# Performance work log

Hardware: AMD Instinct MI355X
Metric: run time of the kernel (lower is better)

The kernel has to match this reference:

```python
import jax, jax.numpy as jnp
import numpy as np

K = 16
H = 128

def _gelu(x):
    return jax.nn.gelu(x, approximate=False)  # torch nn.GELU default (erf)

def _knn_idx(xyz, k):
    # squared pairwise distances; topk of squared dist == topk of cdist (monotone)
    sq = jnp.sum(xyz * xyz, axis=-1)  # [B,N]
    d2 = sq[:, :, None] + sq[:, None, :] - 2.0 * jnp.einsum('bnd,bmd->bnm', xyz, xyz)
    n = xyz.shape[1]
    d2 = d2.at[:, jnp.arange(n), jnp.arange(n)].set(-1.0)  # force self first
    _, idx = jax.lax.top_k(-d2, min(k + 1, n))  # smallest distances
    return idx[..., 1:]  # drop self -> [B,N,K]

def _gather(feat, idx):
    # feat [B,N,C], idx [B,N,K] -> [B,N,K,C]
    return jax.vmap(lambda f, i: f[i])(feat, idx)

def setup_inputs() -> dict:
    key = jax.random.key(0)
    ks = jax.random.split(key, 13)
    s = 0.05
    return {
        'points': jax.random.normal(ks[0], (4, 4096, 6), jnp.float32),
        'Wc1': jax.random.normal(ks[1], (3, H), jnp.float32) * s,
        'bc1': jnp.zeros((H,), jnp.float32),
        'Wc2': jax.random.normal(ks[2], (H, H), jnp.float32) * s,
        'bc2': jnp.zeros((H,), jnp.float32),
        'Wn1': jax.random.normal(ks[3], (4, H), jnp.float32) * s,
        'bn1': jnp.zeros((H,), jnp.float32),
        'Wn2': jax.random.normal(ks[4], (H, H), jnp.float32) * s,
        'bn2': jnp.zeros((H,), jnp.float32),
        'Wo1': jax.random.normal(ks[5], (2 * H, H), jnp.float32) * s,
        'bo1': jnp.zeros((H,), jnp.float32),
        'Wo2': jax.random.normal(ks[6], (H, H), jnp.float32) * s,
        'bo2': jnp.zeros((H,), jnp.float32),
        'k': K,
    }

def reference(points, Wc1, bc1, Wc2, bc2, Wn1, bn1, Wn2, bn2, Wo1, bo1, Wo2, bo2, k):
    xyz = points[..., :3]
    normals = points[..., 3:6]
    idx = jax.lax.stop_gradient(_knn_idx(xyz, k))  # [B,N,K]

    # coord branch: relative neighbor coords -> MLP -> max over K
    rel_xyz = _gather(xyz, idx) - xyz[:, :, None, :]          # [B,N,K,3]
    h = _gelu(rel_xyz @ Wc1 + bc1) @ Wc2 + bc2                # [B,N,K,H]
    coord_feat = jnp.max(h, axis=2)                           # [B,N,H]

    # normal branch: neighbor normals + 1 - cos variation
    neigh_n = _gather(normals, idx)                           # [B,N,K,3]
    variation = 1.0 - jnp.sum(normals[:, :, None, :] * neigh_n, axis=-1, keepdims=True)
    nin = jnp.concatenate([neigh_n, variation], axis=-1)      # [B,N,K,4]
    g = _gelu(nin @ Wn1 + bn1) @ Wn2 + bn2                    # [B,N,K,H]
    normal_feat = jnp.max(g, axis=2)                          # [B,N,H]

    cat = jnp.concatenate([coord_feat, normal_feat], axis=-1) # [B,N,2H]
    return _gelu(cat @ Wo1 + bo1) @ Wo2 + bo2                 # [B,N,H]
```

## Files before the change

kernel.cpp:

```cpp
#include <hip/hip_runtime.h>
#include <math.h>

#define BATCH 4
#define NPTS 4096
#define KNBR 16
#define HDIM 128

typedef __attribute__((ext_vector_type(8))) short bf16x8;
typedef __attribute__((ext_vector_type(4))) float f32x4;
typedef unsigned long long u64;

#define WSOFF_W (1u << 20)
#define WC_HI 0
#define WC_LO 16384
#define WN_HI 32768
#define WN_LO 49152
#define WO1_HI 65536
#define WO1_LO 98304
#define WO2_HI 131072
#define WO2_LO 147456

__device__ __forceinline__ float gelu_f(float x) {
    const float z = x * 0.7071067811865476f;
    const float u = fabsf(z);
    const float z2 = z * z;
    const float t = __builtin_amdgcn_rcpf(fmaf(0.3275911f, u, 1.0f));
    const float E = __expf(-z2);
    float p = fmaf(t, 1.061405429f, -1.453152027f);
    p = fmaf(t, p, 1.421413741f);
    p = fmaf(t, p, -0.284496736f);
    p = fmaf(t, p, 0.254829592f);
    p = p * t;
    const float e = fmaf(-p, E, 1.0f);
    const float hx = 0.5f * x;
    return fmaf(fabsf(hx), e, hx);
}

__device__ __forceinline__ void bsplit(float x, short& hi, short& lo) {
    const unsigned u = __float_as_uint(x);
    hi = (short)(u >> 16);
    const float r = x - __uint_as_float(u & 0xffff0000u);
    lo = (short)(__float_as_uint(r) >> 16);
}

__device__ __forceinline__ u64 readlane_u64(u64 v, int src) {
    const unsigned lo = (unsigned)__builtin_amdgcn_readlane((int)(unsigned)v, src);
    const unsigned hi = (unsigned)__builtin_amdgcn_readlane((int)(unsigned)(v >> 32), src);
    return ((u64)hi << 32) | lo;
}

__global__ __launch_bounds__(256) void prep_points(const float* __restrict__ pts,
                                                   float4* __restrict__ ctab) {
    const int e = blockIdx.x * 256 + threadIdx.x;
    const float* __restrict__ p = pts + (size_t)e * 6;
    const float x = p[0], y = p[1], z = p[2];
    const float sq = x * x + y * y + z * z;
    ctab[e] = make_float4(x, y, z, sq);
}

__global__ __launch_bounds__(256) void prep_weights(
    const float* __restrict__ Wc2, const float* __restrict__ Wn2,
    const float* __restrict__ Wo1, const float* __restrict__ Wo2,
    unsigned short* __restrict__ wbuf)
{
    const int e = blockIdx.x * 256 + threadIdx.x;
    const float* src;
    unsigned short *dh, *dl;
    int idx;
    if (e < 16384)      { src = Wc2; dh = wbuf + WC_HI;  dl = wbuf + WC_LO;  idx = e; }
    else if (e < 32768) { src = Wn2; dh = wbuf + WN_HI;  dl = wbuf + WN_LO;  idx = e - 16384; }
    else if (e < 65536) { src = Wo1; dh = wbuf + WO1_HI; dl = wbuf + WO1_LO; idx = e - 32768; }
    else                { src = Wo2; dh = wbuf + WO2_HI; dl = wbuf + WO2_LO; idx = e - 65536; }
    const int j = idx & 7;
    const int l = (idx >> 3) & 63;
    const int tile = idx >> 9;
    const int ct = tile & 7;
    const int ks = tile >> 3;
    const int n = (l & 15) + 16 * ct;
    const int k = ks * 32 + ((l >> 4) << 3) + j;
    const float x = src[k * 128 + n];
    short hi, lo;
    bsplit(x, hi, lo);
    dh[idx] = (unsigned short)hi;
    dl[idx] = (unsigned short)lo;
}

__global__ __launch_bounds__(256) void knn_kernel(const float4* __restrict__ ctab,
                                                  int* __restrict__ idx_out) {
    const int wq = blockIdx.x * 4 + (threadIdx.x >> 6);
    const int b = wq >> 12;
    const int n = wq & (NPTS - 1);
    const int lane = threadIdx.x & 63;
    const float4* __restrict__ cb = ctab + (size_t)b * NPTS;

    const float4 q = cb[n];

    u64 run = ~0ull;
    u64 cur16max = ~0ull;

    for (int c = 0; c < NPTS / 64; ++c) {
        const int m = lane + 64 * c;
        const float4 cc = cb[m];
        const float dot = q.x * cc.x + q.y * cc.y + q.z * cc.z;
        float d2 = (q.w + cc.w) - 2.0f * dot;
        d2 = fmaxf(d2, 0.0f);
        u64 key = ((u64)__float_as_uint(d2) << 32) | (unsigned)m;
        if (m == n) key = ~0ull;

        u64 mask = __ballot(key < cur16max);
        while (mask) {
            const int src = (int)__builtin_ctzll(mask);
            const u64 K = readlane_u64(key, src);
            u64 prev = __shfl_up(run, 1, 64);
            if (lane == 0) prev = 0;
            run = (run < K) ? run : ((prev < K) ? K : prev);
            cur16max = readlane_u64(run, 15);
            mask &= mask - 1;
            mask &= __ballot(key < cur16max);
        }
    }

    if (lane < KNBR)
        idx_out[((size_t)b * NPTS + n) * KNBR + lane] = (int)(run & 0xffffffffull);
}

template<int NIN>
__device__ __forceinline__ void branch_compute(
    const float (* __restrict__ inp)[4],
    const float* __restrict__ w1s,
    const float* __restrict__ b1s,
    const float* __restrict__ b2s,
    const unsigned short* __restrict__ w2hi,
    const unsigned short* __restrict__ w2lo,
    unsigned short (* __restrict__ catH)[264],
    unsigned short (* __restrict__ catL)[264],
    int colbase, int w, int l)
{
    const int lr = l & 15;
    const int lq = l >> 4;
    const int kb = lq * 8;

    bf16x8 ah[4][2], al[4][2];
#pragma unroll
    for (int ks = 0; ks < 4; ++ks) {
        const int c0 = ks * 32 + kb;
        float wr[NIN][8], bb[8];
#pragma unroll
        for (int d = 0; d < NIN; ++d) {
            *(float4*)&wr[d][0] = *(const float4*)(w1s + (d << 7) + c0);
            *(float4*)&wr[d][4] = *(const float4*)(w1s + (d << 7) + c0 + 4);
        }
        *(float4*)&bb[0] = *(const float4*)(b1s + c0);
        *(float4*)&bb[4] = *(const float4*)(b1s + c0 + 4);
#pragma unroll
        for (int rt = 0; rt < 2; ++rt) {
            const int row = 32 * w + 16 * rt + lr;
            const float4 rv = *(const float4*)&inp[row][0];
#pragma unroll
            for (int jj = 0; jj < 8; ++jj) {
                float x = bb[jj] + rv.x * wr[0][jj] + rv.y * wr[1][jj] + rv.z * wr[2][jj];
                if (NIN == 4) x += rv.w * wr[3][jj];
                x = gelu_f(x);
                short hi, lo;
                bsplit(x, hi, lo);
                ah[ks][rt][jj] = hi;
                al[ks][rt][jj] = lo;
            }
        }
    }

#pragma unroll
    for (int ct = 0; ct < 8; ++ct) {
        f32x4 acc[2];
        acc[0] = (f32x4){0.f, 0.f, 0.f, 0.f};
        acc[1] = (f32x4){0.f, 0.f, 0.f, 0.f};
#pragma unroll
        for (int ks = 0; ks < 4; ++ks) {
            const size_t off = ((size_t)((ks * 8 + ct) * 64 + l)) * 8;
            const bf16x8 bh = *(const bf16x8*)(w2hi + off);
            const bf16x8 bl = *(const bf16x8*)(w2lo + off);
#pragma unroll
            for (int rt = 0; rt < 2; ++rt) {
                acc[rt] = __builtin_amdgcn_mfma_f32_16x16x32_bf16(ah[ks][rt], bh, acc[rt], 0, 0, 0);
                acc[rt] = __builtin_amdgcn_mfma_f32_16x16x32_bf16(ah[ks][rt], bl, acc[rt], 0, 0, 0);
                acc[rt] = __builtin_amdgcn_mfma_f32_16x16x32_bf16(al[ks][rt], bh, acc[rt], 0, 0, 0);
            }
        }
#pragma unroll
        for (int rt = 0; rt < 2; ++rt) {
            const int p = 2 * w + rt;
            const f32x4 a = acc[rt];
            float m = fmaxf(fmaxf(a[0], a[1]), fmaxf(a[2], a[3]));
            m = fmaxf(m, __shfl_xor(m, 16));
            m = fmaxf(m, __shfl_xor(m, 32));
            const int col = lr + 16 * ct;
            const float v = m + b2s[col];
            if (lq == 0) {
                short hi, lo;
                bsplit(v, hi, lo);
                catH[p][colbase + col] = (unsigned short)hi;
                catL[p][colbase + col] = (unsigned short)lo;
            }
        }
    }
}

__global__ __launch_bounds__(256, 4) void mlp_mfma(
    const float* __restrict__ pts, const int* __restrict__ knn_idx,
    const float* __restrict__ Wc1, const float* __restrict__ bc1,
    const float* __restrict__ bc2,
    const float* __restrict__ Wn1, const float* __restrict__ bn1,
    const float* __restrict__ bn2,
    const float* __restrict__ bo1, const float* __restrict__ bo2,
    const unsigned short* __restrict__ wbuf,
    float* __restrict__ outp)
{
    __shared__ __align__(16) float rel[128][4];
    __shared__ __align__(16) float nin[128][4];
    __shared__ float qpt[8][6];
    __shared__ __align__(16) unsigned short catH[8][264];
    __shared__ __align__(16) unsigned short catL[8][264];
    __shared__ __align__(16) unsigned short o1H[8][136];
    __shared__ __align__(16) unsigned short o1L[8][136];
    __shared__ __align__(16) float w1c[3 * 128];
    __shared__ __align__(16) float w1n[4 * 128];
    __shared__ __align__(16) float b1c[128], b2c[128], b1n[128], b2n[128], bo1s[128], bo2s[128];

    const int t = threadIdx.x;
    const int w = t >> 6;
    const int l = t & 63;
    const int lr = l & 15;
    const int lq = l >> 4;
    const int kb = lq * 8;
    const int blk = blockIdx.x;
    const int b = blk >> 9;
    const int n0 = (blk & 511) * 8;
    const float* __restrict__ base = pts + (size_t)b * NPTS * 6;

    for (int i = t; i < 384; i += 256) w1c[i] = Wc1[i];
    for (int i = t; i < 512; i += 256) w1n[i] = Wn1[i];
    if (t < 128) {
        b1c[t] = bc1[t]; b2c[t] = bc2[t];
        b1n[t] = bn1[t]; b2n[t] = bn2[t];
        bo1s[t] = bo1[t]; bo2s[t] = bo2[t];
    }
    if (t < 48) qpt[t / 6][t % 6] = base[(size_t)(n0 + t / 6) * 6 + (t % 6)];
    __syncthreads();
    if (t < 128) {
        const int p = t >> 4;
        const int m = knn_idx[((size_t)b * NPTS + n0 + p) * KNBR + (t & 15)];
        const float cx = base[(size_t)m * 6 + 0];
        const float cy = base[(size_t)m * 6 + 1];
        const float cz = base[(size_t)m * 6 + 2];
        const float nx = base[(size_t)m * 6 + 3];
        const float ny = base[(size_t)m * 6 + 4];
        const float nz = base[(size_t)m * 6 + 5];
        rel[t][0] = cx - qpt[p][0];
        rel[t][1] = cy - qpt[p][1];
        rel[t][2] = cz - qpt[p][2];
        rel[t][3] = 0.0f;
        nin[t][0] = nx; nin[t][1] = ny; nin[t][2] = nz;
        nin[t][3] = 1.0f - (qpt[p][3] * nx + qpt[p][4] * ny + qpt[p][5] * nz);
    }
    __syncthreads();

    branch_compute<3>(rel, w1c, b1c, b2c, wbuf + WC_HI, wbuf + WC_LO,
                      catH, catL, 0, w, l);
    branch_compute<4>(nin, w1n, b1n, b2n, wbuf + WN_HI, wbuf + WN_LO,
                      catH, catL, 128, w, l);
    __syncthreads();

    {
        f32x4 a1[2];
        a1[0] = (f32x4){0.f, 0.f, 0.f, 0.f};
        a1[1] = (f32x4){0.f, 0.f, 0.f, 0.f};
#pragma unroll
        for (int ks = 0; ks < 8; ++ks) {
            const int c0 = ks * 32 + kb;
            const bf16x8 ah = *(const bf16x8*)&catH[lr & 7][c0];
            const bf16x8 al = *(const bf16x8*)&catL[lr & 7][c0];
#pragma unroll
            for (int c2 = 0; c2 < 2; ++c2) {
                const int ct = 2 * w + c2;
                const unsigned short* wp = wbuf + WO1_HI + ((size_t)((ks * 8 + ct) * 64 + l)) * 8;
                const bf16x8 bh = *(const bf16x8*)wp;
                const bf16x8 bl = *(const bf16x8*)(wp + (WO1_LO - WO1_HI));
                a1[c2] = __builtin_amdgcn_mfma_f32_16x16x32_bf16(ah, bh, a1[c2], 0, 0, 0);
                a1[c2] = __builtin_amdgcn_mfma_f32_16x16x32_bf16(ah, bl, a1[c2], 0, 0, 0);
                a1[c2] = __builtin_amdgcn_mfma_f32_16x16x32_bf16(al, bh, a1[c2], 0, 0, 0);
            }
        }
#pragma unroll
        for (int c2 = 0; c2 < 2; ++c2) {
            const int col = lr + 16 * (2 * w + c2);
            const float bo = bo1s[col];
#pragma unroll
            for (int r = 0; r < 4; ++r) {
                const int prow = lq * 4 + r;
                if (prow < 8) {
                    const float x = gelu_f(a1[c2][r] + bo);
                    short hi, lo;
                    bsplit(x, hi, lo);
                    o1H[prow][col] = (unsigned short)hi;
                    o1L[prow][col] = (unsigned short)lo;
                }
            }
        }
    }
    __syncthreads();
    {
        f32x4 a2[2];
        a2[0] = (f32x4){0.f, 0.f, 0.f, 0.f};
        a2[1] = (f32x4){0.f, 0.f, 0.f, 0.f};
#pragma unroll
        for (int ks = 0; ks < 4; ++ks) {
            const int c0 = ks * 32 + kb;
            const bf16x8 ah = *(const bf16x8*)&o1H[lr & 7][c0];
            const bf16x8 al = *(const bf16x8*)&o1L[lr & 7][c0];
#pragma unroll
            for (int c2 = 0; c2 < 2; ++c2) {
                const int ct = 2 * w + c2;
                const unsigned short* wp = wbuf + WO2_HI + ((size_t)((ks * 8 + ct) * 64 + l)) * 8;
                const bf16x8 bh = *(const bf16x8*)wp;
                const bf16x8 bl = *(const bf16x8*)(wp + (WO2_LO - WO2_HI));
                a2[c2] = __builtin_amdgcn_mfma_f32_16x16x32_bf16(ah, bh, a2[c2], 0, 0, 0);
                a2[c2] = __builtin_amdgcn_mfma_f32_16x16x32_bf16(ah, bl, a2[c2], 0, 0, 0);
                a2[c2] = __builtin_amdgcn_mfma_f32_16x16x32_bf16(al, bh, a2[c2], 0, 0, 0);
            }
        }
#pragma unroll
        for (int c2 = 0; c2 < 2; ++c2) {
            const int col = lr + 16 * (2 * w + c2);
            const float bo = bo2s[col];
#pragma unroll
            for (int r = 0; r < 4; ++r) {
                const int prow = lq * 4 + r;
                if (prow < 8)
                    outp[((size_t)b * NPTS + n0 + prow) * HDIM + col] = a2[c2][r] + bo;
            }
        }
    }
}

extern "C" void kernel_launch(void* const* d_in, const int* in_sizes, int n_in,
                              void* d_out, int out_size, void* d_ws, size_t ws_size,
                              hipStream_t stream) {
    const float* pts = (const float*)d_in[0];
    const float* Wc1 = (const float*)d_in[1];
    const float* bc1 = (const float*)d_in[2];
    const float* Wc2 = (const float*)d_in[3];
    const float* bc2 = (const float*)d_in[4];
    const float* Wn1 = (const float*)d_in[5];
    const float* bn1 = (const float*)d_in[6];
    const float* Wn2 = (const float*)d_in[7];
    const float* bn2 = (const float*)d_in[8];
    const float* Wo1 = (const float*)d_in[9];
    const float* bo1 = (const float*)d_in[10];
    const float* Wo2 = (const float*)d_in[11];
    const float* bo2 = (const float*)d_in[12];
    float* outp = (float*)d_out;
    int* idx = (int*)d_ws;
    float4* ctab = (float4*)((char*)d_ws + WSOFF_W);
    unsigned short* wbuf = (unsigned short*)((char*)d_ws + WSOFF_W);

    prep_points<<<dim3(BATCH * NPTS / 256), dim3(256), 0, stream>>>(pts, ctab);
    knn_kernel<<<dim3(BATCH * NPTS / 4), dim3(256), 0, stream>>>(ctab, idx);
    prep_weights<<<dim3(320), dim3(256), 0, stream>>>(Wc2, Wn2, Wo1, Wo2, wbuf);
    mlp_mfma<<<dim3(BATCH * NPTS / 8), dim3(256), 0, stream>>>(
        pts, idx, Wc1, bc1, bc2, Wn1, bn1, bn2, bo1, bo2, wbuf, outp);
}
```

Baseline: 203.1 us.

## Process two query points per wavefront in KNN and restructure branch MFMA loop order

The KNN kernel now has each wavefront handle two query points. Their sorted top-16 lists sit in lanes 0-15 and 16-31 of the same register, so each candidate tile load is shared and the grid is halved. Separately, the branch MLP loop is reordered to compute GELU activations per k-slice and accumulate all 8 column tiles at once. This avoids keeping all A fragments live but holds 16 accumulators instead. The insertion loops stay serial per query, and the register pressure of the new accumulator layout may hurt occupancy under the 4-blocks launch bound.

```diff
diff --git a/kernel.cpp b/kernel.cpp
--- a/kernel.cpp
+++ b/kernel.cpp
@@ -88,40 +88,60 @@
 __global__ __launch_bounds__(256) void knn_kernel(const float4* __restrict__ ctab,
                                                   int* __restrict__ idx_out) {
     const int wq = blockIdx.x * 4 + (threadIdx.x >> 6);
-    const int b = wq >> 12;
-    const int n = wq & (NPTS - 1);
+    const int n0 = (wq * 2) & (NPTS - 1);
+    const int n1 = n0 + 1;
+    const int b = (wq * 2) >> 12;
     const int lane = threadIdx.x & 63;
     const float4* __restrict__ cb = ctab + (size_t)b * NPTS;
 
-    const float4 q = cb[n];
+    const float4 q0 = cb[n0];
+    const float4 q1 = cb[n1];
 
     u64 run = ~0ull;
-    u64 cur16max = ~0ull;
+    u64 max0 = ~0ull, max1 = ~0ull;
 
     for (int c = 0; c < NPTS / 64; ++c) {
         const int m = lane + 64 * c;
         const float4 cc = cb[m];
-        const float dot = q.x * cc.x + q.y * cc.y + q.z * cc.z;
-        float d2 = (q.w + cc.w) - 2.0f * dot;
-        d2 = fmaxf(d2, 0.0f);
-        u64 key = ((u64)__float_as_uint(d2) << 32) | (unsigned)m;
-        if (m == n) key = ~0ull;
-
-        u64 mask = __ballot(key < cur16max);
-        while (mask) {
-            const int src = (int)__builtin_ctzll(mask);
-            const u64 K = readlane_u64(key, src);
+        const float d0 = q0.x * cc.x + q0.y * cc.y + q0.z * cc.z;
+        const float d1 = q1.x * cc.x + q1.y * cc.y + q1.z * cc.z;
+        float e0 = fmaxf((q0.w + cc.w) - 2.0f * d0, 0.0f);
+        float e1 = fmaxf((q1.w + cc.w) - 2.0f * d1, 0.0f);
+        u64 key0 = ((u64)__float_as_uint(e0) << 32) | (unsigned)m;
+        u64 key1 = ((u64)__float_as_uint(e1) << 32) | (unsigned)m;
+        if (m == n0) key0 = ~0ull;
+        if (m == n1) key1 = ~0ull;
+
+        u64 mask0 = __ballot(key0 < max0);
+        while (mask0) {
+            const int src = (int)__builtin_ctzll(mask0);
+            const u64 K = readlane_u64(key0, src);
             u64 prev = __shfl_up(run, 1, 64);
-            if (lane == 0) prev = 0;
-            run = (run < K) ? run : ((prev < K) ? K : prev);
-            cur16max = readlane_u64(run, 15);
-            mask &= mask - 1;
-            mask &= __ballot(key < cur16max);
+            if ((lane & 15) == 0) prev = 0;
+            const u64 cand = (run < K) ? run : ((prev < K) ? K : prev);
+            if ((lane >> 4) == 0) run = cand;
+            max0 = readlane_u64(run, 15);
+            mask0 &= mask0 - 1;
+            mask0 &= __ballot(key0 < max0);
+        }
+        u64 mask1 = __ballot(key1 < max1);
+        while (mask1) {
+            const int src = (int)__builtin_ctzll(mask1);
+            const u64 K = readlane_u64(key1, src);
+            u64 prev = __shfl_up(run, 1, 64);
+            if ((lane & 15) == 0) prev = 0;
+            const u64 cand = (run < K) ? run : ((prev < K) ? K : prev);
+            if ((lane >> 4) == 1) run = cand;
+            max1 = readlane_u64(run, 31);
+            mask1 &= mask1 - 1;
+            mask1 &= __ballot(key1 < max1);
         }
     }
 
     if (lane < KNBR)
-        idx_out[((size_t)b * NPTS + n) * KNBR + lane] = (int)(run & 0xffffffffull);
+        idx_out[((size_t)b * NPTS + n0) * KNBR + lane] = (int)(run & 0xffffffffull);
+    else if (lane < 2 * KNBR)
+        idx_out[((size_t)b * NPTS + n1) * KNBR + (lane - KNBR)] = (int)(run & 0xffffffffull);
 }
 
 template<int NIN>
@@ -140,8 +160,13 @@
     const int lq = l >> 4;
     const int kb = lq * 8;
 
-    bf16x8 ah[4][2], al[4][2];
-#pragma unroll
+    f32x4 acc[2][8];
+#pragma unroll
+    for (int rt = 0; rt < 2; ++rt)
+#pragma unroll
+        for (int ct = 0; ct < 8; ++ct)
+            acc[rt][ct] = (f32x4){0.f, 0.f, 0.f, 0.f};
+
     for (int ks = 0; ks < 4; ++ks) {
         const int c0 = ks * 32 + kb;
         float wr[NIN][8], bb[8];
@@ -152,6 +177,8 @@
         }
         *(float4*)&bb[0] = *(const float4*)(b1s + c0);
         *(float4*)&bb[4] = *(const float4*)(b1s + c0 + 4);
+
+        bf16x8 ah[2], al[2];
 #pragma unroll
         for (int rt = 0; rt < 2; ++rt) {
             const int row = 32 * w + 16 * rt + lr;
@@ -163,33 +190,29 @@
                 x = gelu_f(x);
                 short hi, lo;
                 bsplit(x, hi, lo);
-                ah[ks][rt][jj] = hi;
-                al[ks][rt][jj] = lo;
-            }
-        }
-    }
-
-#pragma unroll
-    for (int ct = 0; ct < 8; ++ct) {
-        f32x4 acc[2];
-        acc[0] = (f32x4){0.f, 0.f, 0.f, 0.f};
-        acc[1] = (f32x4){0.f, 0.f, 0.f, 0.f};
-#pragma unroll
-        for (int ks = 0; ks < 4; ++ks) {
+                ah[rt][jj] = hi;
+                al[rt][jj] = lo;
+            }
+        }
+#pragma unroll
+        for (int ct = 0; ct < 8; ++ct) {
             const size_t off = ((size_t)((ks * 8 + ct) * 64 + l)) * 8;
             const bf16x8 bh = *(const bf16x8*)(w2hi + off);
             const bf16x8 bl = *(const bf16x8*)(w2lo + off);
 #pragma unroll
             for (int rt = 0; rt < 2; ++rt) {
-                acc[rt] = __builtin_amdgcn_mfma_f32_16x16x32_bf16(ah[ks][rt], bh, acc[rt], 0, 0, 0);
-                acc[rt] = __builtin_amdgcn_mfma_f32_16x16x32_bf16(ah[ks][rt], bl, acc[rt], 0, 0, 0);
-                acc[rt] = __builtin_amdgcn_mfma_f32_16x16x32_bf16(al[ks][rt], bh, acc[rt], 0, 0, 0);
-            }
-        }
-#pragma unroll
-        for (int rt = 0; rt < 2; ++rt) {
-            const int p = 2 * w + rt;
-            const f32x4 a = acc[rt];
+                acc[rt][ct] = __builtin_amdgcn_mfma_f32_16x16x32_bf16(ah[rt], bh, acc[rt][ct], 0, 0, 0);
+                acc[rt][ct] = __builtin_amdgcn_mfma_f32_16x16x32_bf16(ah[rt], bl, acc[rt][ct], 0, 0, 0);
+                acc[rt][ct] = __builtin_amdgcn_mfma_f32_16x16x32_bf16(al[rt], bh, acc[rt][ct], 0, 0, 0);
+            }
+        }
+    }
+#pragma unroll
+    for (int rt = 0; rt < 2; ++rt) {
+        const int p = 2 * w + rt;
+#pragma unroll
+        for (int ct = 0; ct < 8; ++ct) {
+            const f32x4 a = acc[rt][ct];
             float m = fmaxf(fmaxf(a[0], a[1]), fmaxf(a[2], a[3]));
             m = fmaxf(m, __shfl_xor(m, 16));
             m = fmaxf(m, __shfl_xor(m, 32));
@@ -364,7 +387,7 @@
     unsigned short* wbuf = (unsigned short*)((char*)d_ws + WSOFF_W);
 
     prep_points<<<dim3(BATCH * NPTS / 256), dim3(256), 0, stream>>>(pts, ctab);
-    knn_kernel<<<dim3(BATCH * NPTS / 4), dim3(256), 0, stream>>>(ctab, idx);
+    knn_kernel<<<dim3(BATCH * NPTS / 8), dim3(256), 0, stream>>>(ctab, idx);
     prep_weights<<<dim3(320), dim3(256), 0, stream>>>(Wc2, Wn2, Wo1, Wo2, wbuf);
     mlp_mfma<<<dim3(BATCH * NPTS / 8), dim3(256), 0, stream>>>(
         pts, idx, Wc1, bc1, bc2, Wn1, bn1, bn2, bo1, bo2, wbuf, outp);
```

Result: no change. 201.7 us (-0.7%).
